# Kernel tuning notes

Hardware: AMD Instinct MI355X
Metric: run time of the kernel (lower is better)

The kernel has to match this reference:

```python
import jax, jax.numpy as jnp
import numpy as np

D_MODEL = 768
H = 12
D_K = D_MODEL // H
B = 2
S = 2048
NEG = -1e9


def setup_inputs() -> dict:
    key = jax.random.key(0)
    ks = jax.random.split(key, 12)
    scale = 1.0 / np.sqrt(D_MODEL)
    inp = {
        "q": jax.random.normal(ks[0], (B, S, D_MODEL), jnp.float32),
        "k": jax.random.normal(ks[1], (B, S, D_MODEL), jnp.float32),
        "v": jax.random.normal(ks[2], (B, S, D_MODEL), jnp.float32),
        "mask": jax.random.randint(ks[3], (B, 1, S, S), 0, 2, jnp.int32),
        "Wq": jax.random.normal(ks[4], (D_MODEL, D_MODEL), jnp.float32) * scale,
        "bq": jnp.zeros((D_MODEL,), jnp.float32),
        "Wk": jax.random.normal(ks[5], (D_MODEL, D_MODEL), jnp.float32) * scale,
        "bk": jnp.zeros((D_MODEL,), jnp.float32),
        "Wv": jax.random.normal(ks[6], (D_MODEL, D_MODEL), jnp.float32) * scale,
        "bv": jnp.zeros((D_MODEL,), jnp.float32),
        "Wo": jax.random.normal(ks[7], (D_MODEL, D_MODEL), jnp.float32) * scale,
        "bo": jnp.zeros((D_MODEL,), jnp.float32),
    }
    return inp


def _split_heads(x):
    # [B, S, D] -> [B, H, S, D_K]
    b, s, _ = x.shape
    return x.reshape(b, s, H, D_K).transpose(0, 2, 1, 3)


def reference(q, k, v, mask, Wq, bq, Wk, bk, Wv, bv, Wo, bo):
    # torch Linear: x @ W.T + b
    query = _split_heads(q @ Wq.T + bq)
    key_ = _split_heads(k @ Wk.T + bk)
    value = _split_heads(v @ Wv.T + bv)

    scores = jnp.einsum("bhqd,bhkd->bhqk", query, key_) / np.sqrt(D_K)
    scores = jnp.where(mask == 0, NEG, scores)
    attn = jax.nn.softmax(scores, axis=-1)  # dropout p=0.0 -> identity

    x = jnp.einsum("bhqk,bhkd->bhqd", attn, value)
    x = x.transpose(0, 2, 1, 3).reshape(q.shape[0], -1, D_MODEL)
    return x @ Wo.T + bo
```

## Files before the change

kernel.cpp:

```cpp
#include <hip/hip_runtime.h>
#include <math.h>

#define DMODEL 768
#define NHEAD 12
#define DKDIM 64
#define BB 2
#define SS 2048
#define MROWS (BB * SS)
#define WELEM (DMODEL * DMODEL)
#define MWORDS (SS / 64)
#define NIT (SS / 64)

typedef unsigned short bf16_t;
typedef __attribute__((ext_vector_type(8))) short s8;
typedef __attribute__((ext_vector_type(4))) float f4;

#define MFMA(a, b, c) __builtin_amdgcn_mfma_f32_16x16x32_bf16((a), (b), (c), 0, 0, 0)

__device__ __forceinline__ bf16_t f2bf(float f) {
    unsigned u = __float_as_uint(f);
    u += 0x7fffu + ((u >> 16) & 1u);
    return (bf16_t)(u >> 16);
}
__device__ __forceinline__ unsigned cvtpk2(float a, float b) {
    unsigned r;
    asm("v_cvt_pk_bf16_f32 %0, %1, %2" : "=v"(r) : "v"(a), "v"(b));
    return r;
}
__device__ __forceinline__ s8 ldfrag(const bf16_t* p) {
    union { uint4 u; s8 s; } x;
    x.u = *(const uint4*)p;
    return x.s;
}
__device__ __forceinline__ void gload16(const bf16_t* g, bf16_t* l) {
    __builtin_amdgcn_global_load_lds(
        (__attribute__((address_space(1))) void*)g,
        (__attribute__((address_space(3))) void*)l,
        16, 0, 0);
}

__device__ __forceinline__ void ld_stage(const bf16_t* p, uint4& u0, uint4& u1) {
    u0 = *(const uint4*)p;
    u1 = *(const uint4*)(p + 8);
}

__global__ void cvt_weights(const float* __restrict__ W0, const float* __restrict__ W1,
                            const float* __restrict__ W2, const float* __restrict__ W3,
                            bf16_t* __restrict__ dst)
{
    const float* src = (blockIdx.y == 0) ? W0 : (blockIdx.y == 1) ? W1
                     : (blockIdx.y == 2) ? W2 : W3;
    bf16_t* d = dst + (size_t)blockIdx.y * WELEM;
    const int i = (blockIdx.x * 256 + threadIdx.x) * 4;
    const float4 v = *(const float4*)(src + i);
    ushort4 h;
    h.x = f2bf(v.x); h.y = f2bf(v.y); h.z = f2bf(v.z); h.w = f2bf(v.w);
    *(ushort4*)(d + i) = h;
}

__global__ __launch_bounds__(256) void cvt_inputs(
    const float* __restrict__ A0, const float* __restrict__ A1,
    const float* __restrict__ A2, bf16_t* __restrict__ dst)
{
    const float* src = (blockIdx.y == 0) ? A0 : (blockIdx.y == 1) ? A1 : A2;
    bf16_t* d = dst + (size_t)blockIdx.y * MROWS * DMODEL;
    const int i = (blockIdx.x * 256 + threadIdx.x) * 4;
    const float4 v = *(const float4*)(src + i);
    ushort4 h;
    h.x = f2bf(v.x); h.y = f2bf(v.y); h.z = f2bf(v.z); h.w = f2bf(v.w);
    *(ushort4*)(d + i) = h;
}

__global__ __launch_bounds__(256) void mask_to_bits(
    const int* __restrict__ mask, unsigned long long* __restrict__ mbits)
{
    const size_t gid = (size_t)blockIdx.x * 256 + threadIdx.x;
    const int m = mask[gid];
    const unsigned long long bal = __ballot(m != 0);
    if ((threadIdx.x & 63) == 0) mbits[gid >> 6] = bal;
}

__global__ __launch_bounds__(256) void gemm_qkv(
    const bf16_t* __restrict__ A0, const bf16_t* __restrict__ A1, const bf16_t* __restrict__ A2,
    const bf16_t* __restrict__ W0, const bf16_t* __restrict__ W1, const bf16_t* __restrict__ W2,
    const float* __restrict__ bias0, const float* __restrict__ bias1, const float* __restrict__ bias2,
    bf16_t* __restrict__ C0, bf16_t* __restrict__ C1, bf16_t* __restrict__ C2,
    float sc0, float sc1, float sc2)
{
    __shared__ uint4 As4[128 * 4];
    __shared__ uint4 Bs4[128 * 4];

    const int z = blockIdx.z;
    const bf16_t* A    = (z == 0) ? A0 : (z == 1) ? A1 : A2;
    const bf16_t* W    = (z == 0) ? W0 : (z == 1) ? W1 : W2;
    const float*  bias = (z == 0) ? bias0 : (z == 1) ? bias1 : bias2;
    bf16_t*       C    = (z == 0) ? C0 : (z == 1) ? C1 : C2;
    const float   sc   = (z == 0) ? sc0 : (z == 1) ? sc1 : sc2;

    const int tid  = threadIdx.x;
    const int lane = tid & 63;
    const int w    = tid >> 6;
    const int wm   = w & 1;
    const int wn   = w >> 1;
    const int l15  = lane & 15;
    const int quad = lane >> 4;
    const int m0   = blockIdx.y * 128;
    const int n0   = blockIdx.x * 128;

    const int r0 = tid >> 2,         s0 = (tid & 3) ^ (r0 & 3);
    const int r1 = 64 + (tid >> 2),  s1 = (tid & 3) ^ (r1 & 3);
    const bf16_t* aS0 = A + (size_t)(m0 + r0) * DMODEL + s0 * 8;
    const bf16_t* aS1 = A + (size_t)(m0 + r1) * DMODEL + s1 * 8;
    const bf16_t* wS0 = W + (size_t)(n0 + r0) * DMODEL + s0 * 8;
    const bf16_t* wS1 = W + (size_t)(n0 + r1) * DMODEL + s1 * 8;
    bf16_t* aD0 = (bf16_t*)As4 + w * 512;
    bf16_t* aD1 = (bf16_t*)As4 + 2048 + w * 512;
    bf16_t* bD0 = (bf16_t*)Bs4 + w * 512;
    bf16_t* bD1 = (bf16_t*)Bs4 + 2048 + w * 512;

    f4 acc[4][4];
    #pragma unroll
    for (int i = 0; i < 4; i++)
        #pragma unroll
        for (int j = 0; j < 4; j++)
            acc[i][j] = (f4){0.f, 0.f, 0.f, 0.f};

    for (int k0 = 0; k0 < DMODEL; k0 += 32) {
        __syncthreads();
        gload16(aS0 + k0, aD0);
        gload16(aS1 + k0, aD1);
        gload16(wS0 + k0, bD0);
        gload16(wS1 + k0, bD1);
        __syncthreads();

        s8 af[4], bf[4];
        #pragma unroll
        for (int t = 0; t < 4; t++) {
            const int ar = wm * 64 + t * 16 + l15;
            const int br = wn * 64 + t * 16 + l15;
            union { uint4 u; s8 s; } xa, xb;
            xa.u = As4[ar * 4 + (quad ^ (ar & 3))];
            xb.u = Bs4[br * 4 + (quad ^ (br & 3))];
            af[t] = xa.s;
            bf[t] = xb.s;
        }
        #pragma unroll
        for (int mt = 0; mt < 4; mt++)
            #pragma unroll
            for (int nt = 0; nt < 4; nt++)
                acc[mt][nt] = MFMA(af[mt], bf[nt], acc[mt][nt]);
    }

    #pragma unroll
    for (int mt = 0; mt < 4; mt++) {
        #pragma unroll
        for (int nt = 0; nt < 4; nt++) {
            const int col = n0 + wn * 64 + nt * 16 + l15;
            const float bb = bias[col];
            #pragma unroll
            for (int reg = 0; reg < 4; reg++) {
                const int row = m0 + wm * 64 + mt * 16 + quad * 4 + reg;
                C[(size_t)row * DMODEL + col] = f2bf((acc[mt][nt][reg] + bb) * sc);
            }
        }
    }
}

__global__ __launch_bounds__(256) void gemm_out(
    const bf16_t* __restrict__ A, const bf16_t* __restrict__ W,
    const float* __restrict__ bias, float* __restrict__ C)
{
    __shared__ uint4 As4[128 * 4];
    __shared__ uint4 Bs4[128 * 4];

    const int tid  = threadIdx.x;
    const int lane = tid & 63;
    const int w    = tid >> 6;
    const int wm   = w & 1;
    const int wn   = w >> 1;
    const int l15  = lane & 15;
    const int quad = lane >> 4;
    const int m0   = blockIdx.y * 128;
    const int n0   = blockIdx.x * 128;

    const int srow  = tid >> 1;
    const int shalf = tid & 1;
    const int sw    = srow & 3;

    const bf16_t* aptr = A + (size_t)(m0 + srow) * DMODEL + shalf * 16;
    const bf16_t* wptr = W + (size_t)(n0 + srow) * DMODEL + shalf * 16;

    f4 acc[4][4];
    #pragma unroll
    for (int i = 0; i < 4; i++)
        #pragma unroll
        for (int j = 0; j < 4; j++)
            acc[i][j] = (f4){0.f, 0.f, 0.f, 0.f};

    for (int k0 = 0; k0 < DMODEL; k0 += 32) {
        uint4 au0, au1, bu0, bu1;
        ld_stage(aptr + k0, au0, au1);
        ld_stage(wptr + k0, bu0, bu1);
        __syncthreads();
        As4[srow * 4 + ((shalf * 2 + 0) ^ sw)] = au0;
        As4[srow * 4 + ((shalf * 2 + 1) ^ sw)] = au1;
        Bs4[srow * 4 + ((shalf * 2 + 0) ^ sw)] = bu0;
        Bs4[srow * 4 + ((shalf * 2 + 1) ^ sw)] = bu1;
        __syncthreads();

        s8 af[4], bf[4];
        #pragma unroll
        for (int t = 0; t < 4; t++) {
            const int ar = wm * 64 + t * 16 + l15;
            const int br = wn * 64 + t * 16 + l15;
            union { uint4 u; s8 s; } xa, xb;
            xa.u = As4[ar * 4 + (quad ^ (ar & 3))];
            xb.u = Bs4[br * 4 + (quad ^ (br & 3))];
            af[t] = xa.s;
            bf[t] = xb.s;
        }
        #pragma unroll
        for (int mt = 0; mt < 4; mt++)
            #pragma unroll
            for (int nt = 0; nt < 4; nt++)
                acc[mt][nt] = MFMA(af[mt], bf[nt], acc[mt][nt]);
    }

    #pragma unroll
    for (int mt = 0; mt < 4; mt++) {
        #pragma unroll
        for (int nt = 0; nt < 4; nt++) {
            const int col = n0 + wn * 64 + nt * 16 + l15;
            const float bb = bias[col];
            #pragma unroll
            for (int reg = 0; reg < 4; reg++) {
                const int row = m0 + wm * 64 + mt * 16 + quad * 4 + reg;
                C[(size_t)row * DMODEL + col] = acc[mt][nt][reg] + bb;
            }
        }
    }
}

__global__ __launch_bounds__(256) void attn_mfma(
    const bf16_t* __restrict__ Q, const bf16_t* __restrict__ K,
    const bf16_t* __restrict__ V, const unsigned long long* __restrict__ mbits,
    bf16_t* __restrict__ O)
{
    __shared__ unsigned Vs[2][64][36];
    __shared__ unsigned Ps[4][16][36];

    const int tid  = threadIdx.x;
    const int lane = tid & 63;
    const int w    = tid >> 6;
    const int l15  = lane & 15;
    const int quad = lane >> 4;
    const int q0   = blockIdx.x * 64;
    const int h    = blockIdx.y;
    const int b    = blockIdx.z;
    const size_t base = ((size_t)b * SS) * DMODEL + (size_t)h * DKDIM;

    const bf16_t* qrow = Q + base + (size_t)(q0 + w * 16 + l15) * DMODEL + quad * 8;
    const s8 qf0 = ldfrag(qrow);
    const s8 qf1 = ldfrag(qrow + 32);

    f4 oacc[4];
    float l_part[4];
    #pragma unroll
    for (int i = 0; i < 4; i++) {
        oacc[i] = (f4){0.f, 0.f, 0.f, 0.f};
        l_part[i] = 0.0f;
    }

    const int kp  = tid & 31;
    const int oct = tid >> 5;
    const bf16_t* vbase = V + base + (size_t)(2 * kp) * DMODEL + oct * 8;
    const bf16_t* kbase = K + base + (size_t)l15 * DMODEL + quad * 8;

    const unsigned long long* mbase =
        mbits + ((size_t)b * SS + (q0 + w * 16 + quad * 4)) * MWORDS;

    uint4 va = *(const uint4*)(vbase);
    uint4 vb = *(const uint4*)(vbase + DMODEL);
    {
        const unsigned short* pa = (const unsigned short*)&va;
        const unsigned short* pb = (const unsigned short*)&vb;
        #pragma unroll
        for (int i = 0; i < 8; i++)
            Vs[0][oct * 8 + i][kp] = (unsigned)pa[i] | ((unsigned)pb[i] << 16);
    }
    va = *(const uint4*)(vbase + (size_t)64 * DMODEL);
    vb = *(const uint4*)(vbase + (size_t)64 * DMODEL + DMODEL);

    s8 kf0[4], kf1[4];
    unsigned long long mw[4];
    #pragma unroll
    for (int nt = 0; nt < 4; nt++) {
        const bf16_t* krow = kbase + (size_t)(nt * 16) * DMODEL;
        kf0[nt] = ldfrag(krow);
        kf1[nt] = ldfrag(krow + 32);
    }
    #pragma unroll
    for (int reg = 0; reg < 4; reg++)
        mw[reg] = mbase[(size_t)reg * MWORDS];

    __syncthreads();

    for (int it = 0; it < NIT; ++it) {
        const int k0  = it * 64;
        const int cur = it & 1;

        if (it + 1 < NIT) {
            const unsigned short* pa = (const unsigned short*)&va;
            const unsigned short* pb = (const unsigned short*)&vb;
            #pragma unroll
            for (int i = 0; i < 8; i++)
                Vs[cur ^ 1][oct * 8 + i][kp] = (unsigned)pa[i] | ((unsigned)pb[i] << 16);
            if (it + 2 < NIT) {
                va = *(const uint4*)(vbase + (size_t)(k0 + 128) * DMODEL);
                vb = *(const uint4*)(vbase + (size_t)(k0 + 128) * DMODEL + DMODEL);
            }
        }

        f4 sacc[4];
        __builtin_amdgcn_s_setprio(1);
        #pragma unroll
        for (int nt = 0; nt < 4; nt++) {
            f4 zz = {0.f, 0.f, 0.f, 0.f};
            zz = MFMA(qf0, kf0[nt], zz);
            zz = MFMA(qf1, kf1[nt], zz);
            sacc[nt] = zz;
        }
        __builtin_amdgcn_s_setprio(0);

        unsigned long long mwc[4];
        #pragma unroll
        for (int reg = 0; reg < 4; reg++) mwc[reg] = mw[reg];
        if (it + 1 < NIT) {
            #pragma unroll
            for (int nt = 0; nt < 4; nt++) {
                const bf16_t* krow = kbase + (size_t)(k0 + 64 + nt * 16) * DMODEL;
                kf0[nt] = ldfrag(krow);
                kf1[nt] = ldfrag(krow + 32);
            }
            #pragma unroll
            for (int reg = 0; reg < 4; reg++)
                mw[reg] = mbase[(size_t)reg * MWORDS + it + 1];
        }

        #pragma unroll
        for (int reg = 0; reg < 4; reg++) {
            const unsigned mlo = ((unsigned)mwc[reg]) >> l15;
            const unsigned mhi = ((unsigned)(mwc[reg] >> 32)) >> l15;
            float p[4];
            p[0] = (mlo & 1u)       ? __builtin_exp2f(sacc[0][reg]) : 0.0f;
            p[1] = (mlo & 0x10000u) ? __builtin_exp2f(sacc[1][reg]) : 0.0f;
            p[2] = (mhi & 1u)       ? __builtin_exp2f(sacc[2][reg]) : 0.0f;
            p[3] = (mhi & 0x10000u) ? __builtin_exp2f(sacc[3][reg]) : 0.0f;
            l_part[reg] += (p[0] + p[1]) + (p[2] + p[3]);

            #pragma unroll
            for (int nt = 0; nt < 4; nt++) {
                const float mine  = p[nt];
                const float other = __shfl_xor(mine, 1, 16);
                if ((lane & 1) == 0)
                    Ps[w][quad * 4 + reg][nt * 8 + (l15 >> 1)] = cvtpk2(mine, other);
            }
        }

        __builtin_amdgcn_s_setprio(1);
        #pragma unroll
        for (int kt = 0; kt < 2; kt++) {
            union { uint4 u; s8 s; } pf;
            pf.u = *(const uint4*)&Ps[w][l15][kt * 16 + quad * 4];
            #pragma unroll
            for (int dt = 0; dt < 4; dt++) {
                union { uint4 u; s8 s; } vf;
                vf.u = *(const uint4*)&Vs[cur][dt * 16 + l15][kt * 16 + quad * 4];
                oacc[dt] = MFMA(pf.s, vf.s, oacc[dt]);
            }
        }
        __builtin_amdgcn_s_setprio(0);

        __syncthreads();
    }

    #pragma unroll
    for (int reg = 0; reg < 4; reg++) {
        float rs = l_part[reg];
        rs += __shfl_xor(rs, 1, 16);
        rs += __shfl_xor(rs, 2, 16);
        rs += __shfl_xor(rs, 4, 16);
        rs += __shfl_xor(rs, 8, 16);
        const float inv = 1.0f / rs;
        const size_t row = q0 + w * 16 + quad * 4 + reg;
        #pragma unroll
        for (int dt = 0; dt < 4; dt++) {
            O[base + row * DMODEL + dt * 16 + l15] = f2bf(oacc[dt][reg] * inv);
        }
    }
}

extern "C" void kernel_launch(void* const* d_in, const int* in_sizes, int n_in,
                              void* d_out, int out_size, void* d_ws, size_t ws_size,
                              hipStream_t stream)
{
    const float* q    = (const float*)d_in[0];
    const float* k    = (const float*)d_in[1];
    const float* v    = (const float*)d_in[2];
    const int*   mask = (const int*)  d_in[3];
    const float* Wq   = (const float*)d_in[4];
    const float* bq   = (const float*)d_in[5];
    const float* Wk   = (const float*)d_in[6];
    const float* bk   = (const float*)d_in[7];
    const float* Wv   = (const float*)d_in[8];
    const float* bv   = (const float*)d_in[9];
    const float* Wo   = (const float*)d_in[10];
    const float* bo   = (const float*)d_in[11];
    float* out = (float*)d_out;

    bf16_t* wsb = (bf16_t*)d_ws;
    const size_t plane = (size_t)MROWS * DMODEL;
    bf16_t* Qp  = wsb;
    bf16_t* Kp  = wsb + plane;
    bf16_t* Vp  = wsb + 2 * plane;
    bf16_t* Ctx = wsb + 3 * plane;
    bf16_t* Wqb = wsb + 4 * plane;
    bf16_t* Wkb = Wqb + WELEM;
    bf16_t* Wvb = Wkb + WELEM;
    bf16_t* Wob = Wvb + WELEM;
    bf16_t* Abf = Wob + WELEM;
    unsigned long long* mbits = (unsigned long long*)(Abf + 3 * plane);

    cvt_weights<<<dim3(WELEM / 1024, 4), 256, 0, stream>>>(Wq, Wk, Wv, Wo, Wqb);
    cvt_inputs<<<dim3((int)(plane / 1024), 3), 256, 0, stream>>>(q, k, v, Abf);
    mask_to_bits<<<dim3((BB * SS * SS) / 256), 256, 0, stream>>>(mask, mbits);

    gemm_qkv<<<dim3(DMODEL / 128, MROWS / 128, 3), 256, 0, stream>>>(
        Abf, Abf + plane, Abf + 2 * plane, Wqb, Wkb, Wvb, bq, bk, bv,
        Qp, Kp, Vp, 0.125f * 1.44269504f, 1.0f, 1.0f);

    attn_mfma<<<dim3(SS / 64, NHEAD, BB), 256, 0, stream>>>(Qp, Kp, Vp, mbits, Ctx);

    gemm_out<<<dim3(DMODEL / 128, MROWS / 128), 256, 0, stream>>>(Ctx, Wob, bo, out);
}
```

Before: 332.6 us.

## Widen GEMM K-tiles to 64 and keep attention P in registers

Both projection GEMMs now stage 64-wide K tiles with an 8-way XOR swizzle, which halves the number of barrier pairs per block. The attention kernel swaps the MFMA operand order so S^T lands with one query row per lane. The P fragment for the PV MFMA is then built through cross-lane shuffles instead of a shared-memory round trip, and the mask becomes one word per lane. This removes the Ps LDS buffer and its stores, at the cost of more shuffles and register pressure.

```diff
diff --git a/kernel.cpp b/kernel.cpp
--- a/kernel.cpp
+++ b/kernel.cpp
@@ -39,11 +39,6 @@
         16, 0, 0);
 }
 
-__device__ __forceinline__ void ld_stage(const bf16_t* p, uint4& u0, uint4& u1) {
-    u0 = *(const uint4*)p;
-    u1 = *(const uint4*)(p + 8);
-}
-
 __global__ void cvt_weights(const float* __restrict__ W0, const float* __restrict__ W1,
                             const float* __restrict__ W2, const float* __restrict__ W3,
                             bf16_t* __restrict__ dst)
@@ -87,8 +82,8 @@
     bf16_t* __restrict__ C0, bf16_t* __restrict__ C1, bf16_t* __restrict__ C2,
     float sc0, float sc1, float sc2)
 {
-    __shared__ uint4 As4[128 * 4];
-    __shared__ uint4 Bs4[128 * 4];
+    __shared__ bf16_t As[128 * 64];
+    __shared__ bf16_t Bs[128 * 64];
 
     const int z = blockIdx.z;
     const bf16_t* A    = (z == 0) ? A0 : (z == 1) ? A1 : A2;
@@ -107,16 +102,10 @@
     const int m0   = blockIdx.y * 128;
     const int n0   = blockIdx.x * 128;
 
-    const int r0 = tid >> 2,         s0 = (tid & 3) ^ (r0 & 3);
-    const int r1 = 64 + (tid >> 2),  s1 = (tid & 3) ^ (r1 & 3);
-    const bf16_t* aS0 = A + (size_t)(m0 + r0) * DMODEL + s0 * 8;
-    const bf16_t* aS1 = A + (size_t)(m0 + r1) * DMODEL + s1 * 8;
-    const bf16_t* wS0 = W + (size_t)(n0 + r0) * DMODEL + s0 * 8;
-    const bf16_t* wS1 = W + (size_t)(n0 + r1) * DMODEL + s1 * 8;
-    bf16_t* aD0 = (bf16_t*)As4 + w * 512;
-    bf16_t* aD1 = (bf16_t*)As4 + 2048 + w * 512;
-    bf16_t* bD0 = (bf16_t*)Bs4 + w * 512;
-    bf16_t* bD1 = (bf16_t*)Bs4 + 2048 + w * 512;
+    const int lrow = lane >> 3;
+    const int lblk = (lane & 7) ^ lrow;
+    const bf16_t* aS = A + (size_t)(m0 + w * 8 + lrow) * DMODEL + lblk * 8;
+    const bf16_t* wS = W + (size_t)(n0 + w * 8 + lrow) * DMODEL + lblk * 8;
 
     f4 acc[4][4];
     #pragma unroll
@@ -125,30 +114,32 @@
         for (int j = 0; j < 4; j++)
             acc[i][j] = (f4){0.f, 0.f, 0.f, 0.f};
 
-    for (int k0 = 0; k0 < DMODEL; k0 += 32) {
+    for (int k0 = 0; k0 < DMODEL; k0 += 64) {
         __syncthreads();
-        gload16(aS0 + k0, aD0);
-        gload16(aS1 + k0, aD1);
-        gload16(wS0 + k0, bD0);
-        gload16(wS1 + k0, bD1);
+        #pragma unroll
+        for (int i = 0; i < 4; i++) {
+            gload16(aS + (size_t)(i * 32) * DMODEL + k0, As + (i * 256 + w * 64) * 8);
+            gload16(wS + (size_t)(i * 32) * DMODEL + k0, Bs + (i * 256 + w * 64) * 8);
+        }
         __syncthreads();
 
-        s8 af[4], bf[4];
-        #pragma unroll
-        for (int t = 0; t < 4; t++) {
-            const int ar = wm * 64 + t * 16 + l15;
-            const int br = wn * 64 + t * 16 + l15;
-            union { uint4 u; s8 s; } xa, xb;
-            xa.u = As4[ar * 4 + (quad ^ (ar & 3))];
-            xb.u = Bs4[br * 4 + (quad ^ (br & 3))];
-            af[t] = xa.s;
-            bf[t] = xb.s;
-        }
-        #pragma unroll
-        for (int mt = 0; mt < 4; mt++)
-            #pragma unroll
-            for (int nt = 0; nt < 4; nt++)
-                acc[mt][nt] = MFMA(af[mt], bf[nt], acc[mt][nt]);
+        #pragma unroll
+        for (int kk = 0; kk < 2; kk++) {
+            s8 af[4], bf[4];
+            #pragma unroll
+            for (int t = 0; t < 4; t++) {
+                const int ar  = wm * 64 + t * 16 + l15;
+                const int br  = wn * 64 + t * 16 + l15;
+                const int blk = (kk * 4 + quad) ^ (l15 & 7);
+                af[t] = ldfrag(As + ar * 64 + blk * 8);
+                bf[t] = ldfrag(Bs + br * 64 + blk * 8);
+            }
+            #pragma unroll
+            for (int mt = 0; mt < 4; mt++)
+                #pragma unroll
+                for (int nt = 0; nt < 4; nt++)
+                    acc[mt][nt] = MFMA(af[mt], bf[nt], acc[mt][nt]);
+        }
     }
 
     #pragma unroll
@@ -170,8 +161,8 @@
     const bf16_t* __restrict__ A, const bf16_t* __restrict__ W,
     const float* __restrict__ bias, float* __restrict__ C)
 {
-    __shared__ uint4 As4[128 * 4];
-    __shared__ uint4 Bs4[128 * 4];
+    __shared__ bf16_t As[128 * 64];
+    __shared__ bf16_t Bs[128 * 64];
 
     const int tid  = threadIdx.x;
     const int lane = tid & 63;
@@ -183,12 +174,12 @@
     const int m0   = blockIdx.y * 128;
     const int n0   = blockIdx.x * 128;
 
-    const int srow  = tid >> 1;
-    const int shalf = tid & 1;
-    const int sw    = srow & 3;
-
-    const bf16_t* aptr = A + (size_t)(m0 + srow) * DMODEL + shalf * 16;
-    const bf16_t* wptr = W + (size_t)(n0 + srow) * DMODEL + shalf * 16;
+    const int srow = tid >> 1;
+    const int sh   = tid & 1;
+    const int sw7  = srow & 7;
+
+    const bf16_t* aptr = A + (size_t)(m0 + srow) * DMODEL + sh * 32;
+    const bf16_t* wptr = W + (size_t)(n0 + srow) * DMODEL + sh * 32;
 
     f4 acc[4][4];
     #pragma unroll
@@ -197,33 +188,39 @@
         for (int j = 0; j < 4; j++)
             acc[i][j] = (f4){0.f, 0.f, 0.f, 0.f};
 
-    for (int k0 = 0; k0 < DMODEL; k0 += 32) {
-        uint4 au0, au1, bu0, bu1;
-        ld_stage(aptr + k0, au0, au1);
-        ld_stage(wptr + k0, bu0, bu1);
+    for (int k0 = 0; k0 < DMODEL; k0 += 64) {
+        uint4 au[4], bu[4];
+        #pragma unroll
+        for (int j = 0; j < 4; j++) {
+            au[j] = *(const uint4*)(aptr + k0 + j * 8);
+            bu[j] = *(const uint4*)(wptr + k0 + j * 8);
+        }
         __syncthreads();
-        As4[srow * 4 + ((shalf * 2 + 0) ^ sw)] = au0;
-        As4[srow * 4 + ((shalf * 2 + 1) ^ sw)] = au1;
-        Bs4[srow * 4 + ((shalf * 2 + 0) ^ sw)] = bu0;
-        Bs4[srow * 4 + ((shalf * 2 + 1) ^ sw)] = bu1;
+        #pragma unroll
+        for (int j = 0; j < 4; j++) {
+            const int blk = (sh * 4 + j) ^ sw7;
+            *(uint4*)(As + srow * 64 + blk * 8) = au[j];
+            *(uint4*)(Bs + srow * 64 + blk * 8) = bu[j];
+        }
         __syncthreads();
 
-        s8 af[4], bf[4];
-        #pragma unroll
-        for (int t = 0; t < 4; t++) {
-            const int ar = wm * 64 + t * 16 + l15;
-            const int br = wn * 64 + t * 16 + l15;
-            union { uint4 u; s8 s; } xa, xb;
-            xa.u = As4[ar * 4 + (quad ^ (ar & 3))];
-            xb.u = Bs4[br * 4 + (quad ^ (br & 3))];
-            af[t] = xa.s;
-            bf[t] = xb.s;
-        }
-        #pragma unroll
-        for (int mt = 0; mt < 4; mt++)
-            #pragma unroll
-            for (int nt = 0; nt < 4; nt++)
-                acc[mt][nt] = MFMA(af[mt], bf[nt], acc[mt][nt]);
+        #pragma unroll
+        for (int kk = 0; kk < 2; kk++) {
+            s8 af[4], bf[4];
+            #pragma unroll
+            for (int t = 0; t < 4; t++) {
+                const int ar  = wm * 64 + t * 16 + l15;
+                const int br  = wn * 64 + t * 16 + l15;
+                const int blk = (kk * 4 + quad) ^ (l15 & 7);
+                af[t] = ldfrag(As + ar * 64 + blk * 8);
+                bf[t] = ldfrag(Bs + br * 64 + blk * 8);
+            }
+            #pragma unroll
+            for (int mt = 0; mt < 4; mt++)
+                #pragma unroll
+                for (int nt = 0; nt < 4; nt++)
+                    acc[mt][nt] = MFMA(af[mt], bf[nt], acc[mt][nt]);
+        }
     }
 
     #pragma unroll
@@ -247,7 +244,6 @@
     bf16_t* __restrict__ O)
 {
     __shared__ unsigned Vs[2][64][36];
-    __shared__ unsigned Ps[4][16][36];
 
     const int tid  = threadIdx.x;
     const int lane = tid & 63;
@@ -264,12 +260,9 @@
     const s8 qf1 = ldfrag(qrow + 32);
 
     f4 oacc[4];
-    float l_part[4];
-    #pragma unroll
-    for (int i = 0; i < 4; i++) {
-        oacc[i] = (f4){0.f, 0.f, 0.f, 0.f};
-        l_part[i] = 0.0f;
-    }
+    #pragma unroll
+    for (int i = 0; i < 4; i++) oacc[i] = (f4){0.f, 0.f, 0.f, 0.f};
+    float l_part = 0.0f;
 
     const int kp  = tid & 31;
     const int oct = tid >> 5;
@@ -277,7 +270,11 @@
     const bf16_t* kbase = K + base + (size_t)l15 * DMODEL + quad * 8;
 
     const unsigned long long* mbase =
-        mbits + ((size_t)b * SS + (q0 + w * 16 + quad * 4)) * MWORDS;
+        mbits + ((size_t)b * SS + (q0 + w * 16 + l15)) * MWORDS;
+
+    const int sA  = l15 + (((2 * quad) & 3) << 4);
+    const int sB  = l15 + (((2 * quad + 1) & 3) << 4);
+    const bool hiQ = (quad & 2) != 0;
 
     uint4 va = *(const uint4*)(vbase);
     uint4 vb = *(const uint4*)(vbase + DMODEL);
@@ -292,16 +289,14 @@
     vb = *(const uint4*)(vbase + (size_t)64 * DMODEL + DMODEL);
 
     s8 kf0[4], kf1[4];
-    unsigned long long mw[4];
+    unsigned long long mw;
     #pragma unroll
     for (int nt = 0; nt < 4; nt++) {
         const bf16_t* krow = kbase + (size_t)(nt * 16) * DMODEL;
         kf0[nt] = ldfrag(krow);
         kf1[nt] = ldfrag(krow + 32);
     }
-    #pragma unroll
-    for (int reg = 0; reg < 4; reg++)
-        mw[reg] = mbase[(size_t)reg * MWORDS];
+    mw = mbase[0];
 
     __syncthreads();
 
@@ -326,15 +321,13 @@
         #pragma unroll
         for (int nt = 0; nt < 4; nt++) {
             f4 zz = {0.f, 0.f, 0.f, 0.f};
-            zz = MFMA(qf0, kf0[nt], zz);
-            zz = MFMA(qf1, kf1[nt], zz);
+            zz = MFMA(kf0[nt], qf0, zz);
+            zz = MFMA(kf1[nt], qf1, zz);
             sacc[nt] = zz;
         }
         __builtin_amdgcn_s_setprio(0);
 
-        unsigned long long mwc[4];
-        #pragma unroll
-        for (int reg = 0; reg < 4; reg++) mwc[reg] = mw[reg];
+        const unsigned long long mwc = mw;
         if (it + 1 < NIT) {
             #pragma unroll
             for (int nt = 0; nt < 4; nt++) {
@@ -342,60 +335,65 @@
                 kf0[nt] = ldfrag(krow);
                 kf1[nt] = ldfrag(krow + 32);
             }
-            #pragma unroll
-            for (int reg = 0; reg < 4; reg++)
-                mw[reg] = mbase[(size_t)reg * MWORDS + it + 1];
-        }
-
-        #pragma unroll
-        for (int reg = 0; reg < 4; reg++) {
-            const unsigned mlo = ((unsigned)mwc[reg]) >> l15;
-            const unsigned mhi = ((unsigned)(mwc[reg] >> 32)) >> l15;
-            float p[4];
-            p[0] = (mlo & 1u)       ? __builtin_exp2f(sacc[0][reg]) : 0.0f;
-            p[1] = (mlo & 0x10000u) ? __builtin_exp2f(sacc[1][reg]) : 0.0f;
-            p[2] = (mhi & 1u)       ? __builtin_exp2f(sacc[2][reg]) : 0.0f;
-            p[3] = (mhi & 0x10000u) ? __builtin_exp2f(sacc[3][reg]) : 0.0f;
-            l_part[reg] += (p[0] + p[1]) + (p[2] + p[3]);
-
-            #pragma unroll
-            for (int nt = 0; nt < 4; nt++) {
-                const float mine  = p[nt];
-                const float other = __shfl_xor(mine, 1, 16);
-                if ((lane & 1) == 0)
-                    Ps[w][quad * 4 + reg][nt * 8 + (l15 >> 1)] = cvtpk2(mine, other);
-            }
-        }
-
-        __builtin_amdgcn_s_setprio(1);
+            mw = mbase[it + 1];
+        }
+
+        const unsigned ml = ((unsigned)mwc) >> (quad * 4);
+        const unsigned mh = ((unsigned)(mwc >> 32)) >> (quad * 4);
+        unsigned wlo[4], whi[4];
+        #pragma unroll
+        for (int nt = 0; nt < 4; nt++) {
+            const unsigned mm = (nt & 2) ? mh : ml;
+            const int shft = (nt & 1) * 16;
+            const float p0 = ((mm >> (shft + 0)) & 1u) ? __builtin_exp2f(sacc[nt][0]) : 0.0f;
+            const float p1 = ((mm >> (shft + 1)) & 1u) ? __builtin_exp2f(sacc[nt][1]) : 0.0f;
+            const float p2 = ((mm >> (shft + 2)) & 1u) ? __builtin_exp2f(sacc[nt][2]) : 0.0f;
+            const float p3 = ((mm >> (shft + 3)) & 1u) ? __builtin_exp2f(sacc[nt][3]) : 0.0f;
+            l_part += (p0 + p1) + (p2 + p3);
+            wlo[nt] = cvtpk2(p0, p1);
+            whi[nt] = cvtpk2(p2, p3);
+        }
+
         #pragma unroll
         for (int kt = 0; kt < 2; kt++) {
+            const unsigned a0 = (unsigned)__shfl((int)wlo[2 * kt],     sA, 64);
+            const unsigned a1 = (unsigned)__shfl((int)wlo[2 * kt + 1], sA, 64);
+            const unsigned b0 = (unsigned)__shfl((int)whi[2 * kt],     sA, 64);
+            const unsigned b1 = (unsigned)__shfl((int)whi[2 * kt + 1], sA, 64);
+            const unsigned c0 = (unsigned)__shfl((int)wlo[2 * kt],     sB, 64);
+            const unsigned c1 = (unsigned)__shfl((int)wlo[2 * kt + 1], sB, 64);
+            const unsigned d0 = (unsigned)__shfl((int)whi[2 * kt],     sB, 64);
+            const unsigned d1 = (unsigned)__shfl((int)whi[2 * kt + 1], sB, 64);
             union { uint4 u; s8 s; } pf;
-            pf.u = *(const uint4*)&Ps[w][l15][kt * 16 + quad * 4];
+            pf.u.x = hiQ ? a1 : a0;
+            pf.u.y = hiQ ? b1 : b0;
+            pf.u.z = hiQ ? c1 : c0;
+            pf.u.w = hiQ ? d1 : d0;
+
+            __builtin_amdgcn_s_setprio(1);
             #pragma unroll
             for (int dt = 0; dt < 4; dt++) {
                 union { uint4 u; s8 s; } vf;
                 vf.u = *(const uint4*)&Vs[cur][dt * 16 + l15][kt * 16 + quad * 4];
                 oacc[dt] = MFMA(pf.s, vf.s, oacc[dt]);
             }
-        }
-        __builtin_amdgcn_s_setprio(0);
+            __builtin_amdgcn_s_setprio(0);
+        }
 
         __syncthreads();
     }
 
+    l_part += __shfl_xor(l_part, 16, 64);
+    l_part += __shfl_xor(l_part, 32, 64);
+    const float inv = 1.0f / l_part;
+
     #pragma unroll
     for (int reg = 0; reg < 4; reg++) {
-        float rs = l_part[reg];
-        rs += __shfl_xor(rs, 1, 16);
-        rs += __shfl_xor(rs, 2, 16);
-        rs += __shfl_xor(rs, 4, 16);
-        rs += __shfl_xor(rs, 8, 16);
-        const float inv = 1.0f / rs;
+        const float invq = __shfl(inv, (quad << 4) + quad * 4 + reg, 64);
         const size_t row = q0 + w * 16 + quad * 4 + reg;
         #pragma unroll
         for (int dt = 0; dt < 4; dt++) {
-            O[base + row * DMODEL + dt * 16 + l15] = f2bf(oacc[dt][reg] * inv);
+            O[base + row * DMODEL + dt * 16 + l15] = f2bf(oacc[dt][reg] * invq);
         }
     }
 }
```

After: 337.8 us. No clear change (+1.6%).
